# Performance work log

Hardware: AMD Instinct MI355X
Metric: run time of the kernel (lower is better)

## Reference

```python
import jax, jax.numpy as jnp
import numpy as np

N = 8192   # number of queries
D = 384    # MiniLM-L3 embedding dim
M = 1024   # number of unique docs (segments)


def setup_inputs() -> dict:
    key = jax.random.key(0)
    k1, k2, k3 = jax.random.split(key, 3)
    emb_q = jax.random.normal(k1, (N, D), dtype=jnp.float32)
    label = jax.random.uniform(k2, (N,), dtype=jnp.float32)  # relevance labels, >0 so group sums are nonzero
    doc_ids = jax.random.randint(k3, (N,), 0, M)              # plays the role of unique(emb_k) inverse indices
    return {"emb_q": emb_q, "label": label, "doc_ids": doc_ids}


def reference(emb_q, label, doc_ids):
    # cosine-similarity matrix between queries
    norm_q = emb_q / jnp.linalg.norm(emb_q, axis=1, keepdims=True)   # [N, D]
    sim = norm_q @ norm_q.T                                          # [N_i, N_q]

    # Original double python loop computes, for each doc group j and each row i:
    #   theta[i, q in group j] = sum_{q' in j} label[q'] * sim[i, q'] / sum_{q' in j} label[q']
    # which is a segment-sum over the column axis grouped by doc, then a gather back.
    weighted = sim * label[None, :]                                  # [N_i, N_q]
    num = jax.ops.segment_sum(weighted.T, doc_ids, num_segments=M)   # [M, N_i]
    den = jax.ops.segment_sum(label, doc_ids, num_segments=M)        # [M]
    theta = (num[doc_ids] / den[doc_ids][:, None]).T                 # [N_i, N_q]
    return theta
```

## Files before the change

### kernel.cpp

```cpp
#include <hip/hip_runtime.h>

#define N_Q   8192
#define DIM   384
#define N_DOC 1024

typedef unsigned short ushort_t;
typedef __attribute__((ext_vector_type(8))) short bf16x8;
typedef __attribute__((ext_vector_type(4))) float f32x4;
typedef __attribute__((ext_vector_type(4))) int i32x4;

__device__ __forceinline__ float bf2f(ushort_t u) {
    union { unsigned i; float f; } c; c.i = ((unsigned)u) << 16; return c.f;
}
__device__ __forceinline__ ushort_t f2bf(float f) {
    union { float f; unsigned u; } c; c.f = f;
    unsigned r = c.u + 0x7FFF + ((c.u >> 16) & 1);
    return (ushort_t)(r >> 16);
}
__device__ __forceinline__ void gload_lds16(const void* g, void* l) {
    __builtin_amdgcn_global_load_lds((const __attribute__((address_space(1))) void*)g,
                                     (__attribute__((address_space(3))) void*)l, 16, 0, 0);
}

__global__ __launch_bounds__(256) void k_normalize(const float* __restrict__ emb,
                                                   ushort_t* __restrict__ nqb) {
    int w    = (blockIdx.x * 256 + threadIdx.x) >> 6;
    int lane = threadIdx.x & 63;
    const float* row = emb + (size_t)w * DIM;
    float v[6];
    float ss = 0.f;
#pragma unroll
    for (int r = 0; r < 6; ++r) { v[r] = row[lane + 64 * r]; ss += v[r] * v[r]; }
#pragma unroll
    for (int off = 32; off; off >>= 1) ss += __shfl_xor(ss, off);
    float inv = rsqrtf(ss);
    ushort_t* o = nqb + (size_t)w * DIM;
#pragma unroll
    for (int r = 0; r < 6; ++r) o[lane + 64 * r] = f2bf(v[r] * inv);
}

#define SS_WAVES 8
__global__ __launch_bounds__(512) void k_segsum(const ushort_t* __restrict__ nqb,
                                                const float* __restrict__ label,
                                                const int*   __restrict__ ids,
                                                ushort_t* __restrict__ Hb) {
    __shared__ float pacc[SS_WAVES][DIM];
    __shared__ float pden[SS_WAVES];
    int j    = blockIdx.x;
    int lane = threadIdx.x & 63;
    int w    = threadIdx.x >> 6;
    const int span = N_Q / SS_WAVES;
    int q0 = w * span;

    float acc[6] = {0.f, 0.f, 0.f, 0.f, 0.f, 0.f};
    float den = 0.f;

    int idc = ids[q0 + lane];
    for (int base = q0; base < q0 + span; base += 64) {
        int nb = base + 64;
        int idn = (nb < q0 + span) ? ids[nb + lane] : -1;
        unsigned long long mask = __ballot(idc == j);
        while (mask) {
            int b = __builtin_ctzll(mask);
            mask &= mask - 1;
            int q = base + b;
            float lab = label[q];
            const ushort_t* r = nqb + (size_t)q * DIM;
#pragma unroll
            for (int t = 0; t < 6; ++t) acc[t] = fmaf(lab, bf2f(r[lane + 64 * t]), acc[t]);
            den += lab;
        }
        idc = idn;
    }
#pragma unroll
    for (int t = 0; t < 6; ++t) pacc[w][lane + 64 * t] = acc[t];
    if (lane == 0) pden[w] = den;
    __syncthreads();

    int d = threadIdx.x;
    if (d < DIM) {
        float s = 0.f, dn = 0.f;
#pragma unroll
        for (int ww = 0; ww < SS_WAVES; ++ww) { s += pacc[ww][d]; dn += pden[ww]; }
        float invd = (dn > 0.f) ? (1.f / dn) : 0.f;
        Hb[(size_t)j * DIM + d] = f2bf(s * invd);
    }
}

#define BM 128
#define BN 128
#define BK 64

__global__ __launch_bounds__(256) void k_gemm(const ushort_t* __restrict__ A,
                                              const ushort_t* __restrict__ B,
                                              ushort_t* __restrict__ Tb) {
    __shared__ ushort_t As[BM * BK];
    __shared__ ushort_t Bs[BN * BK];
    int tid  = threadIdx.x;
    int lane = tid & 63, wid = tid >> 6;
    int wr = wid >> 1, wc = wid & 1;
    int row0 = blockIdx.y * BM, col0 = blockIdx.x * BN;
    int fr = lane & 15, kg = lane >> 4;

    f32x4 acc[4][4];
#pragma unroll
    for (int i = 0; i < 4; ++i)
#pragma unroll
        for (int j = 0; j < 4; ++j) acc[i][j] = (f32x4)0.f;

    for (int k0 = 0; k0 < DIM; k0 += BK) {
#pragma unroll
        for (int r = 0; r < 4; ++r) {
            int flat = r * 256 + tid;
            int row = flat >> 3, gd = flat & 7;
            int gs = gd ^ (row & 7);
            int wbase = (r * 256 + wid * 64) * 8;
            gload_lds16(A + (size_t)(row0 + row) * DIM + k0 + gs * 8, &As[wbase]);
            gload_lds16(B + (size_t)(col0 + row) * DIM + k0 + gs * 8, &Bs[wbase]);
        }
        __syncthreads();

#pragma unroll
        for (int ks = 0; ks < 2; ++ks) {
            bf16x8 a[4], b[4];
#pragma unroll
            for (int mi = 0; mi < 4; ++mi) {
                int m = wr * 64 + mi * 16 + fr;
                a[mi] = *(const bf16x8*)&As[m * 64 + (((ks * 4 + kg) ^ (m & 7)) << 3)];
            }
#pragma unroll
            for (int ni = 0; ni < 4; ++ni) {
                int n = wc * 64 + ni * 16 + fr;
                b[ni] = *(const bf16x8*)&Bs[n * 64 + (((ks * 4 + kg) ^ (n & 7)) << 3)];
            }
#pragma unroll
            for (int mi = 0; mi < 4; ++mi)
#pragma unroll
                for (int ni = 0; ni < 4; ++ni)
                    acc[mi][ni] = __builtin_amdgcn_mfma_f32_16x16x32_bf16(a[mi], b[ni], acc[mi][ni], 0, 0, 0);
        }
        __syncthreads();
    }

#pragma unroll
    for (int mi = 0; mi < 4; ++mi)
#pragma unroll
        for (int ni = 0; ni < 4; ++ni)
#pragma unroll
            for (int r = 0; r < 4; ++r)
                Tb[(size_t)(row0 + wr * 64 + mi * 16 + kg * 4 + r) * N_DOC
                   + col0 + wc * 64 + ni * 16 + fr] = f2bf(acc[mi][ni][r]);
}

#define EROWS 8
__global__ __launch_bounds__(256) void k_expand(const ushort_t* __restrict__ Tb,
                                                const int*      __restrict__ ids,
                                                float*          __restrict__ out) {
    __shared__ float trow[EROWS * N_DOC];
    int tid = threadIdx.x;
    int i0  = blockIdx.x * EROWS;

    i32x4 idv[N_Q / 4 / 256];
    const i32x4* id4 = (const i32x4*)ids;
#pragma unroll
    for (int it = 0; it < N_Q / 4 / 256; ++it) idv[it] = id4[it * 256 + tid];

    const bf16x8* Tv = (const bf16x8*)(Tb + (size_t)i0 * N_DOC);
#pragma unroll
    for (int c = 0; c < 4; ++c) {
        int chunk = c * 256 + tid;
        bf16x8 v = Tv[chunk];
        f32x4 lo = { bf2f((ushort_t)v[0]), bf2f((ushort_t)v[1]), bf2f((ushort_t)v[2]), bf2f((ushort_t)v[3]) };
        f32x4 hi = { bf2f((ushort_t)v[4]), bf2f((ushort_t)v[5]), bf2f((ushort_t)v[6]), bf2f((ushort_t)v[7]) };
        *(f32x4*)&trow[chunk * 8]     = lo;
        *(f32x4*)&trow[chunk * 8 + 4] = hi;
    }
    __syncthreads();

#pragma unroll
    for (int it = 0; it < N_Q / 4 / 256; ++it) {
        int q4 = it * 256 + tid;
        i32x4 id = idv[it];
#pragma unroll
        for (int r = 0; r < EROWS; ++r) {
            const float* tr = &trow[r * N_DOC];
            f32x4 v = { tr[id.x], tr[id.y], tr[id.z], tr[id.w] };
            __builtin_nontemporal_store(v, (f32x4*)(out + (size_t)(i0 + r) * N_Q) + q4);
        }
    }
}

extern "C" void kernel_launch(void* const* d_in, const int* in_sizes, int n_in,
                              void* d_out, int out_size, void* d_ws, size_t ws_size,
                              hipStream_t stream) {
    const float* emb   = (const float*)d_in[0];
    const float* label = (const float*)d_in[1];
    const int*   ids   = (const int*)d_in[2];
    float* out = (float*)d_out;

    ushort_t* nqb = (ushort_t*)d_ws;
    ushort_t* Hb  = nqb + (size_t)N_Q * DIM;
    ushort_t* Tb  = Hb + (size_t)N_DOC * DIM;

    k_normalize<<<N_Q / 4, 256, 0, stream>>>(emb, nqb);
    k_segsum<<<N_DOC, 512, 0, stream>>>(nqb, label, ids, Hb);
    k_gemm<<<dim3(N_DOC / BN, N_Q / BM), 256, 0, stream>>>(nqb, Hb, Tb);
    k_expand<<<N_Q / EROWS, 256, 0, stream>>>(Tb, ids, out);
}
```

Baseline: 78.99 us.

## Fuse normalization into segment-sum kernel and double-buffer GEMM LDS tiles

```diff
diff --git a/kernel.cpp b/kernel.cpp
--- a/kernel.cpp
+++ b/kernel.cpp
@@ -22,28 +22,12 @@
                                      (__attribute__((address_space(3))) void*)l, 16, 0, 0);
 }
 
-__global__ __launch_bounds__(256) void k_normalize(const float* __restrict__ emb,
-                                                   ushort_t* __restrict__ nqb) {
-    int w    = (blockIdx.x * 256 + threadIdx.x) >> 6;
-    int lane = threadIdx.x & 63;
-    const float* row = emb + (size_t)w * DIM;
-    float v[6];
-    float ss = 0.f;
-#pragma unroll
-    for (int r = 0; r < 6; ++r) { v[r] = row[lane + 64 * r]; ss += v[r] * v[r]; }
-#pragma unroll
-    for (int off = 32; off; off >>= 1) ss += __shfl_xor(ss, off);
-    float inv = rsqrtf(ss);
-    ushort_t* o = nqb + (size_t)w * DIM;
-#pragma unroll
-    for (int r = 0; r < 6; ++r) o[lane + 64 * r] = f2bf(v[r] * inv);
-}
-
 #define SS_WAVES 8
-__global__ __launch_bounds__(512) void k_segsum(const ushort_t* __restrict__ nqb,
-                                                const float* __restrict__ label,
-                                                const int*   __restrict__ ids,
-                                                ushort_t* __restrict__ Hb) {
+__global__ __launch_bounds__(512) void k_segnorm(const float* __restrict__ emb,
+                                                 const float* __restrict__ label,
+                                                 const int*   __restrict__ ids,
+                                                 ushort_t* __restrict__ nqb,
+                                                 ushort_t* __restrict__ Hb) {
     __shared__ float pacc[SS_WAVES][DIM];
     __shared__ float pden[SS_WAVES];
     int j    = blockIdx.x;
@@ -65,9 +49,21 @@
             mask &= mask - 1;
             int q = base + b;
             float lab = label[q];
-            const ushort_t* r = nqb + (size_t)q * DIM;
-#pragma unroll
-            for (int t = 0; t < 6; ++t) acc[t] = fmaf(lab, bf2f(r[lane + 64 * t]), acc[t]);
+            const float* row = emb + (size_t)q * DIM;
+            float v[6];
+            float ss = 0.f;
+#pragma unroll
+            for (int t = 0; t < 6; ++t) { v[t] = row[lane + 64 * t]; ss += v[t] * v[t]; }
+#pragma unroll
+            for (int off = 32; off; off >>= 1) ss += __shfl_xor(ss, off);
+            float inv = rsqrtf(ss);
+            ushort_t* o = nqb + (size_t)q * DIM;
+#pragma unroll
+            for (int t = 0; t < 6; ++t) {
+                float nv = v[t] * inv;
+                acc[t] = fmaf(lab, nv, acc[t]);
+                o[lane + 64 * t] = f2bf(nv);
+            }
             den += lab;
         }
         idc = idn;
@@ -90,35 +86,42 @@
 #define BM 128
 #define BN 128
 #define BK 64
+#define KQ (DIM / BK)
 
 __global__ __launch_bounds__(256) void k_gemm(const ushort_t* __restrict__ A,
                                               const ushort_t* __restrict__ B,
                                               ushort_t* __restrict__ Tb) {
-    __shared__ ushort_t As[BM * BK];
-    __shared__ ushort_t Bs[BN * BK];
+    __shared__ ushort_t As[2][BM * BK];
+    __shared__ ushort_t Bs[2][BN * BK];
     int tid  = threadIdx.x;
     int lane = tid & 63, wid = tid >> 6;
     int wr = wid >> 1, wc = wid & 1;
     int row0 = blockIdx.y * BM, col0 = blockIdx.x * BN;
     int fr = lane & 15, kg = lane >> 4;
 
-    f32x4 acc[4][4];
-#pragma unroll
-    for (int i = 0; i < 4; ++i)
-#pragma unroll
-        for (int j = 0; j < 4; ++j) acc[i][j] = (f32x4)0.f;
-
-    for (int k0 = 0; k0 < DIM; k0 += BK) {
+    auto stage = [&](int kq, int bf) {
 #pragma unroll
         for (int r = 0; r < 4; ++r) {
             int flat = r * 256 + tid;
             int row = flat >> 3, gd = flat & 7;
             int gs = gd ^ (row & 7);
             int wbase = (r * 256 + wid * 64) * 8;
-            gload_lds16(A + (size_t)(row0 + row) * DIM + k0 + gs * 8, &As[wbase]);
-            gload_lds16(B + (size_t)(col0 + row) * DIM + k0 + gs * 8, &Bs[wbase]);
-        }
-        __syncthreads();
+            gload_lds16(A + (size_t)(row0 + row) * DIM + kq * BK + gs * 8, &As[bf][wbase]);
+            gload_lds16(B + (size_t)(col0 + row) * DIM + kq * BK + gs * 8, &Bs[bf][wbase]);
+        }
+    };
+
+    f32x4 acc[4][4];
+#pragma unroll
+    for (int i = 0; i < 4; ++i)
+#pragma unroll
+        for (int j = 0; j < 4; ++j) acc[i][j] = (f32x4)0.f;
+
+    stage(0, 0);
+    __syncthreads();
+    int cur = 0;
+    for (int kq = 0; kq < KQ; ++kq) {
+        if (kq + 1 < KQ) stage(kq + 1, cur ^ 1);
 
 #pragma unroll
         for (int ks = 0; ks < 2; ++ks) {
@@ -126,12 +129,12 @@
 #pragma unroll
             for (int mi = 0; mi < 4; ++mi) {
                 int m = wr * 64 + mi * 16 + fr;
-                a[mi] = *(const bf16x8*)&As[m * 64 + (((ks * 4 + kg) ^ (m & 7)) << 3)];
+                a[mi] = *(const bf16x8*)&As[cur][m * 64 + (((ks * 4 + kg) ^ (m & 7)) << 3)];
             }
 #pragma unroll
             for (int ni = 0; ni < 4; ++ni) {
                 int n = wc * 64 + ni * 16 + fr;
-                b[ni] = *(const bf16x8*)&Bs[n * 64 + (((ks * 4 + kg) ^ (n & 7)) << 3)];
+                b[ni] = *(const bf16x8*)&Bs[cur][n * 64 + (((ks * 4 + kg) ^ (n & 7)) << 3)];
             }
 #pragma unroll
             for (int mi = 0; mi < 4; ++mi)
@@ -140,6 +143,7 @@
                     acc[mi][ni] = __builtin_amdgcn_mfma_f32_16x16x32_bf16(a[mi], b[ni], acc[mi][ni], 0, 0, 0);
         }
         __syncthreads();
+        cur ^= 1;
     }
 
 #pragma unroll
@@ -202,8 +206,7 @@
     ushort_t* Hb  = nqb + (size_t)N_Q * DIM;
     ushort_t* Tb  = Hb + (size_t)N_DOC * DIM;
 
-    k_normalize<<<N_Q / 4, 256, 0, stream>>>(emb, nqb);
-    k_segsum<<<N_DOC, 512, 0, stream>>>(nqb, label, ids, Hb);
+    k_segnorm<<<N_DOC, 512, 0, stream>>>(emb, label, ids, nqb, Hb);
     k_gemm<<<dim3(N_DOC / BN, N_Q / BM), 256, 0, stream>>>(nqb, Hb, Tb);
     k_expand<<<N_Q / EROWS, 256, 0, stream>>>(Tb, ids, out);
 }
```

Result: faster. 75.68 us (-4.2%).
